# Optimization experiments

Measured on AMD Instinct MI355X. Metric: run time of the kernel, lower is better.

Reference implementation:

```python
import jax, jax.numpy as jnp
import numpy as np

N_NODES = 50000
N_EDGES = 800000
N_GRAPHS = 64
IN_CH = 128
HID = 128
PROC_X = 128
Q_DIM = 768
PROC_Q = 128
OUT_CH = 32


def setup_inputs() -> dict:
    key = jax.random.key(0)
    ks = jax.random.split(key, 16)
    inp = {
        "x": jax.random.normal(ks[0], (N_NODES, IN_CH), dtype=jnp.float32),
        "edge_index": jax.random.randint(ks[1], (2, N_EDGES), 0, N_NODES, dtype=jnp.int64),
        "batch": jnp.sort(jax.random.randint(ks[2], (N_NODES,), 0, N_GRAPHS, dtype=jnp.int64)),
        "question_embedding": jax.random.normal(ks[3], (N_GRAPHS, Q_DIM), dtype=jnp.float32),
    }
    s = 1.0 / np.sqrt(HID)
    inp["W0"] = jax.random.uniform(ks[4], (IN_CH, HID), minval=-s, maxval=s)
    inp["b0"] = jnp.zeros((HID,), jnp.float32)
    inp["W1"] = jax.random.uniform(ks[5], (HID, HID), minval=-s, maxval=s)
    inp["b1"] = jnp.zeros((HID,), jnp.float32)
    inp["W2"] = jax.random.uniform(ks[6], (HID, PROC_X), minval=-s, maxval=s)
    inp["b2"] = jnp.zeros((PROC_X,), jnp.float32)
    inp["fc0_w"] = jax.random.uniform(ks[7], (Q_DIM, PROC_Q), minval=-s, maxval=s)
    inp["fc0_b"] = jnp.zeros((PROC_Q,), jnp.float32)
    inp["fc1_w"] = jax.random.uniform(ks[8], (PROC_X + PROC_Q, HID), minval=-s, maxval=s)
    inp["fc1_b"] = jnp.zeros((HID,), jnp.float32)
    inp["fc2_w"] = jax.random.uniform(ks[9], (HID, OUT_CH), minval=-s, maxval=s)
    inp["fc2_b"] = jnp.zeros((OUT_CH,), jnp.float32)
    return inp


def _gcn_norm(edge_index, n_nodes):
    """Add self-loops and compute symmetric GCN normalization per edge."""
    loop = jnp.arange(n_nodes, dtype=edge_index.dtype)
    src = jnp.concatenate([edge_index[0], loop])
    dst = jnp.concatenate([edge_index[1], loop])
    ones = jnp.ones_like(dst, dtype=jnp.float32)
    deg = jax.ops.segment_sum(ones, dst, num_segments=n_nodes)
    dinv = jnp.where(deg > 0, jax.lax.rsqrt(deg), 0.0)
    norm = dinv[src] * dinv[dst]  # [E+N]
    return src, dst, norm


def _gcn_conv(x, src, dst, norm, W, b):
    h = x @ W                                # [N, F_out]
    msg = h[src] * norm[:, None]             # gather + scale  [E+N, F_out]
    agg = jax.ops.segment_sum(msg, dst, num_segments=x.shape[0])
    return agg + b


def reference(x, edge_index, batch, question_embedding,
              W0, b0, W1, b1, W2, b2,
              fc0_w, fc0_b, fc1_w, fc1_b, fc2_w, fc2_b):
    n = x.shape[0]
    src, dst, norm = _gcn_norm(edge_index, n)
    h = jax.nn.relu(_gcn_conv(x, src, dst, norm, W0, b0))
    h = jax.nn.relu(_gcn_conv(h, src, dst, norm, W1, b1))
    h = jax.nn.relu(_gcn_conv(h, src, dst, norm, W2, b2))
    q = jax.nn.relu(question_embedding @ fc0_w + fc0_b)  # [G, PROC_Q]
    q_exp = q[batch]                                      # [N, PROC_Q]
    combined = jnp.concatenate([h, q_exp], axis=1)
    out = jax.nn.relu(combined @ fc1_w + fc1_b)
    out = out @ fc2_w + fc2_b
    return out
```

## Files before the change

kernel.cpp:

```cpp
#include <hip/hip_runtime.h>
#include <hip/hip_bf16.h>

#define N_NODES 50000
#define N_EDGES 800000
#define N_GRAPHS 64
#define LSTR 136

typedef __attribute__((ext_vector_type(4))) short s4v;
typedef __attribute__((ext_vector_type(8))) short s8v;
typedef __attribute__((ext_vector_type(16))) float f16v;

struct HL { short hi, lo; };

__device__ inline HL bsplit(float f) {
    HL r;
    unsigned u = __float_as_uint(f);
    unsigned rh = (u + 0x7FFFu + ((u >> 16) & 1u)) >> 16;
    r.hi = (short)rh;
    float fh = __uint_as_float(rh << 16);
    float fl = f - fh;
    unsigned u2 = __float_as_uint(fl);
    unsigned rl = (u2 + 0x7FFFu + ((u2 >> 16) & 1u)) >> 16;
    r.lo = (short)rl;
    return r;
}

__device__ inline unsigned short f2bf(float f) {
    unsigned u = __float_as_uint(f);
    return (unsigned short)((u + 0x7FFFu + ((u >> 16) & 1u)) >> 16);
}

__device__ inline float bflo(unsigned u) { return __uint_as_float(u << 16); }
__device__ inline float bfhi(unsigned u) { return __uint_as_float(u & 0xFFFF0000u); }


__global__ void k_hist(const int* __restrict__ ei, int* __restrict__ cnt,
                       int* __restrict__ rank, int E) {
    int e = blockIdx.x * 256 + threadIdx.x;
    if (e < E) rank[e] = atomicAdd(&cnt[ei[E + e]], 1);
}

__global__ __launch_bounds__(512) void k_scan_a(const int* __restrict__ cnt,
                                                int* __restrict__ rowptr,
                                                int* __restrict__ bsum,
                                                float* __restrict__ dinv, int n) {
    __shared__ int s[512];
    int t = threadIdx.x;
    int i = blockIdx.x * 512 + t;
    int v = (i < n) ? cnt[i] : 0;
    if (i < n) dinv[i] = rsqrtf((float)(v + 1));
    int pv = (v + 7) & ~7;
    s[t] = pv;
    __syncthreads();
    for (int d = 1; d < 512; d <<= 1) {
        int x = (t >= d) ? s[t - d] : 0;
        __syncthreads();
        s[t] += x;
        __syncthreads();
    }
    if (i < n) rowptr[i] = s[t] - pv;
    if (t == 511) bsum[blockIdx.x] = s[511];
}

__global__ __launch_bounds__(512) void k_scan_c(int* __restrict__ rowptr,
                                                const int* __restrict__ bsum,
                                                int n, int nb) {
    __shared__ int sb[128];
    int t = threadIdx.x;
    if (t < 128) sb[t] = (t < nb) ? bsum[t] : 0;
    __syncthreads();
    for (int d = 1; d < 128; d <<= 1) {
        int x = 0;
        if (t < 128 && t >= d) x = sb[t - d];
        __syncthreads();
        if (t < 128) sb[t] += x;
        __syncthreads();
    }
    int add = (blockIdx.x > 0) ? sb[blockIdx.x - 1] : 0;
    int i = blockIdx.x * 512 + t;
    if (i < n) rowptr[i] += add;
    if (i == 0) rowptr[n] = sb[nb - 1];
}

__global__ void k_fill_csr(const int* __restrict__ ei, const int* __restrict__ rowptr,
                           const int* __restrict__ rank,
                           unsigned short* __restrict__ colA, int E) {
    int e = blockIdx.x * 256 + threadIdx.x;
    if (e >= E) return;
    colA[rowptr[ei[E + e]] + rank[e]] = (unsigned short)ei[e];
}

__global__ __launch_bounds__(512) void k_prep(const float* __restrict__ qe,
                                              const float* __restrict__ fc0w,
                                              const float* __restrict__ fc0b,
                                              const float* __restrict__ fc1w,
                                              const float* __restrict__ fc1b,
                                              const float* __restrict__ W0,
                                              const float* __restrict__ W1,
                                              const float* __restrict__ W2,
                                              const float* __restrict__ fc2w,
                                              short* __restrict__ WH,
                                              short* __restrict__ WL,
                                              int* __restrict__ cntz,
                                              unsigned* __restrict__ Hsd,
                                              unsigned short* __restrict__ colA,
                                              float* __restrict__ qq) {
    int b = blockIdx.x, tid = threadIdx.x;
    if (b >= 225) {
        int idx = (b - 225) * 512 + tid;
        if (idx < 143752) {
            uint4 p;
            p.x = p.y = p.z = p.w = 0xC350C350u;
            ((uint4*)colA)[idx] = p;
        }
        return;
    }
    if (b >= 200) {
        int idx = (b - 200) * 512 + tid;
        if (idx < 12504) ((int4*)cntz)[idx] = make_int4(0, 0, 0, 0);
        if (b == 200 && tid < 64) Hsd[(unsigned)N_NODES * 64u + tid] = 0u;
        return;
    }
    if (b >= 64) {
        int i = (b - 64) * 512 + tid;
        float val;
        int dst;
        if (i < 65536) {
            int mat = i >> 14, off = i & 16383;
            int k = off >> 7, n = off & 127;
            const float* src = (mat == 0) ? W0 : (mat == 1) ? W1 : (mat == 2) ? W2 : fc1w;
            val = src[k * 128 + n];
            dst = mat * 16384 + n * 128 + k;
        } else {
            int off = i - 65536;
            int k = off >> 5, n = off & 31;
            val = fc2w[k * 32 + n];
            dst = 65536 + n * 128 + k;
        }
        HL r = bsplit(val);
        WH[dst] = r.hi;
        WL[dst] = r.lo;
        return;
    }
    __shared__ float qs[768];
    __shared__ float red[512];
    __shared__ float ql[128];
    const float* fc1bot = fc1w + 128 * 128;
    int g = b;
    for (int i = tid; i < 768; i += 512) qs[i] = qe[g * 768 + i];
    __syncthreads();
    int j = tid & 127, sl = tid >> 7;
    int kb = sl * 192;
    float a0 = 0, a1 = 0, a2 = 0, a3 = 0;
    for (int k = 0; k < 192; k += 4) {
        a0 += qs[kb + k + 0] * fc0w[(kb + k + 0) * 128 + j];
        a1 += qs[kb + k + 1] * fc0w[(kb + k + 1) * 128 + j];
        a2 += qs[kb + k + 2] * fc0w[(kb + k + 2) * 128 + j];
        a3 += qs[kb + k + 3] * fc0w[(kb + k + 3) * 128 + j];
    }
    red[tid] = (a0 + a1) + (a2 + a3);
    __syncthreads();
    if (tid < 128)
        ql[tid] = fmaxf(((red[tid] + red[tid + 128]) + (red[tid + 256] + red[tid + 384]))
                        + fc0b[tid], 0.f);
    __syncthreads();
    kb = sl * 32;
    float b0 = 0, b1 = 0;
    for (int k = 0; k < 32; k += 2) {
        b0 += ql[kb + k + 0] * fc1bot[(kb + k + 0) * 128 + j];
        b1 += ql[kb + k + 1] * fc1bot[(kb + k + 1) * 128 + j];
    }
    red[tid] = b0 + b1;
    __syncthreads();
    if (tid < 128)
        qq[g * 128 + tid] = ((red[tid] + red[tid + 128]) + (red[tid + 256] + red[tid + 384]))
                            + fc1b[tid];
}

__global__ __launch_bounds__(256) void k_gather(const unsigned* __restrict__ Hs,
                                                const int* __restrict__ rowptr,
                                                const unsigned short* __restrict__ colA,
                                                const float* __restrict__ dinv,
                                                const float* __restrict__ bias,
                                                unsigned* __restrict__ GH, int n) {
    int node = __builtin_amdgcn_readfirstlane(blockIdx.x * 4 + (threadIdx.x >> 6));
    if (node >= n) return;
    int l = threadIdx.x & 63;
    int e0 = __builtin_amdgcn_readfirstlane(rowptr[node]);
    int e1 = __builtin_amdgcn_readfirstlane(rowptr[node + 1]);
    float a0 = 0.f, a1 = 0.f;
    for (int e = e0; e < e1; e += 8) {
        uint4 cw = *(const uint4*)(colA + e);
        const unsigned* r0 = Hs + (cw.x & 0xFFFFu) * 64u;
        const unsigned* r1 = Hs + (cw.x >> 16) * 64u;
        const unsigned* r2 = Hs + (cw.y & 0xFFFFu) * 64u;
        const unsigned* r3 = Hs + (cw.y >> 16) * 64u;
        const unsigned* r4 = Hs + (cw.z & 0xFFFFu) * 64u;
        const unsigned* r5 = Hs + (cw.z >> 16) * 64u;
        const unsigned* r6 = Hs + (cw.w & 0xFFFFu) * 64u;
        const unsigned* r7 = Hs + (cw.w >> 16) * 64u;
        unsigned u0 = r0[l], u1 = r1[l], u2 = r2[l], u3 = r3[l];
        unsigned u4 = r4[l], u5 = r5[l], u6 = r6[l], u7 = r7[l];
        a0 += ((bflo(u0) + bflo(u1)) + (bflo(u2) + bflo(u3)))
            + ((bflo(u4) + bflo(u5)) + (bflo(u6) + bflo(u7)));
        a1 += ((bfhi(u0) + bfhi(u1)) + (bfhi(u2) + bfhi(u3)))
            + ((bfhi(u4) + bfhi(u5)) + (bfhi(u6) + bfhi(u7)));
    }
    float di = dinv[node];
    unsigned uh = Hs[(unsigned)node * 64u + l];
    float2 bb = ((const float2*)bias)[l];
    float o0 = fmaxf((a0 + bflo(uh)) * di + bb.x, 0.f);
    float o1 = fmaxf((a1 + bfhi(uh)) * di + bb.y, 0.f);
    GH[(unsigned)node * 64u + l] = (unsigned)f2bf(o0) | ((unsigned)f2bf(o1) << 16);
}

template <int SPLITIN>
__global__ __launch_bounds__(128) void gemm_mf(const float* __restrict__ A32,
                                               const unsigned short* __restrict__ GHin,
                                               const short* __restrict__ WTh,
                                               const short* __restrict__ WTl,
                                               const float* __restrict__ dinv,
                                               unsigned short* __restrict__ oHs,
                                               int nrows) {
    __shared__ short Ah[32 * LSTR];
    const int tid = threadIdx.x;
    const int row0 = blockIdx.x * 32;

    if (SPLITIN == 0) {
        #pragma unroll
        for (int i = 0; i < 8; ++i) {
            int u = i * 128 + tid;
            int r = u >> 5, c4 = u & 31;
            int gr = row0 + r;
            float4 v = make_float4(0.f, 0.f, 0.f, 0.f);
            if (gr < nrows) v = ((const float4*)A32)[(size_t)gr * 32 + c4];
            s4v h4 = {(short)f2bf(v.x), (short)f2bf(v.y), (short)f2bf(v.z), (short)f2bf(v.w)};
            *(s4v*)&Ah[r * LSTR + c4 * 4] = h4;
        }
    } else {
        #pragma unroll
        for (int i = 0; i < 4; ++i) {
            int u = i * 128 + tid;
            int r = u >> 4, j = u & 15;
            int gr = row0 + r;
            s8v h8 = {};
            if (gr < nrows) h8 = *(const s8v*)&GHin[(size_t)gr * 128 + j * 8];
            *(s8v*)&Ah[r * LSTR + j * 8] = h8;
        }
    }
    __syncthreads();

    const int wv = tid >> 6, lane = tid & 63;
    const int m = lane & 31, half = lane >> 5;
    const int c0 = wv * 64 + m;
    f16v acc0 = {0.f}, acc1 = {0.f};
    #pragma unroll
    for (int ks = 0; ks < 8; ++ks) {
        int ko = ks * 16 + half * 8;
        s8v ah  = *(const s8v*)&Ah[m * LSTR + ko];
        s8v bh0 = *(const s8v*)&WTh[(size_t)c0 * 128 + ko];
        s8v bl0 = *(const s8v*)&WTl[(size_t)c0 * 128 + ko];
        s8v bh1 = *(const s8v*)&WTh[(size_t)(c0 + 32) * 128 + ko];
        s8v bl1 = *(const s8v*)&WTl[(size_t)(c0 + 32) * 128 + ko];
        acc0 = __builtin_amdgcn_mfma_f32_32x32x16_bf16(ah, bh0, acc0, 0, 0, 0);
        acc0 = __builtin_amdgcn_mfma_f32_32x32x16_bf16(ah, bl0, acc0, 0, 0, 0);
        acc1 = __builtin_amdgcn_mfma_f32_32x32x16_bf16(ah, bh1, acc1, 0, 0, 0);
        acc1 = __builtin_amdgcn_mfma_f32_32x32x16_bf16(ah, bl1, acc1, 0, 0, 0);
    }

    #pragma unroll
    for (int reg = 0; reg < 16; ++reg) {
        int rl = (reg & 3) + 8 * (reg >> 2) + 4 * half;
        int gr = row0 + rl;
        if (gr >= nrows) continue;
        float sc = dinv[gr];
        oHs[(size_t)gr * 128 + c0]      = f2bf(acc0[reg] * sc);
        oHs[(size_t)gr * 128 + c0 + 32] = f2bf(acc1[reg] * sc);
    }
}

__global__ __launch_bounds__(128) void k_fc12(const unsigned short* __restrict__ GHin,
                                              const short* __restrict__ W1h,
                                              const short* __restrict__ W1l,
                                              const short* __restrict__ W2h,
                                              const short* __restrict__ W2l,
                                              const float* __restrict__ qq,
                                              const int* __restrict__ batch,
                                              const float* __restrict__ bias,
                                              float* __restrict__ out, int nrows) {
    __shared__ short Ph[32 * LSTR], Pl[32 * LSTR];
    __shared__ float red[32 * 33];
    const int tid = threadIdx.x;
    const int row0 = blockIdx.x * 32;

    #pragma unroll
    for (int i = 0; i < 4; ++i) {
        int u = i * 128 + tid;
        int r = u >> 4, j = u & 15;
        int gr = row0 + r;
        s8v h8 = {};
        if (gr < nrows) h8 = *(const s8v*)&GHin[(size_t)gr * 128 + j * 8];
        *(s8v*)&Ph[r * LSTR + j * 8] = h8;
    }
    __syncthreads();

    const int wv = tid >> 6, lane = tid & 63;
    const int m = lane & 31, half = lane >> 5;
    const int c0 = wv * 64 + m;
    f16v acc0 = {0.f}, acc1 = {0.f};
    #pragma unroll
    for (int ks = 0; ks < 8; ++ks) {
        int ko = ks * 16 + half * 8;
        s8v ah  = *(const s8v*)&Ph[m * LSTR + ko];
        s8v bh0 = *(const s8v*)&W1h[(size_t)c0 * 128 + ko];
        s8v bl0 = *(const s8v*)&W1l[(size_t)c0 * 128 + ko];
        s8v bh1 = *(const s8v*)&W1h[(size_t)(c0 + 32) * 128 + ko];
        s8v bl1 = *(const s8v*)&W1l[(size_t)(c0 + 32) * 128 + ko];
        acc0 = __builtin_amdgcn_mfma_f32_32x32x16_bf16(ah, bh0, acc0, 0, 0, 0);
        acc0 = __builtin_amdgcn_mfma_f32_32x32x16_bf16(ah, bl0, acc0, 0, 0, 0);
        acc1 = __builtin_amdgcn_mfma_f32_32x32x16_bf16(ah, bh1, acc1, 0, 0, 0);
        acc1 = __builtin_amdgcn_mfma_f32_32x32x16_bf16(ah, bl1, acc1, 0, 0, 0);
    }
    __syncthreads();

    #pragma unroll
    for (int reg = 0; reg < 16; ++reg) {
        int rl = (reg & 3) + 8 * (reg >> 2) + 4 * half;
        int gr = row0 + rl;
        int g = (gr < nrows) ? batch[gr] : 0;
        float q0 = qq[(size_t)g * 128 + c0];
        float q1 = qq[(size_t)g * 128 + c0 + 32];
        float v0 = fmaxf(acc0[reg] + q0, 0.f);
        float v1 = fmaxf(acc1[reg] + q1, 0.f);
        HL p0 = bsplit(v0), p1 = bsplit(v1);
        Ph[rl * LSTR + c0] = p0.hi;
        Pl[rl * LSTR + c0] = p0.lo;
        Ph[rl * LSTR + c0 + 32] = p1.hi;
        Pl[rl * LSTR + c0 + 32] = p1.lo;
    }
    __syncthreads();

    f16v acc2 = {0.f};
    #pragma unroll
    for (int ks = 0; ks < 4; ++ks) {
        int ko = wv * 64 + ks * 16 + half * 8;
        s8v ah = *(const s8v*)&Ph[m * LSTR + ko];
        s8v al = *(const s8v*)&Pl[m * LSTR + ko];
        s8v bh = *(const s8v*)&W2h[(size_t)m * 128 + ko];
        s8v bl = *(const s8v*)&W2l[(size_t)m * 128 + ko];
        acc2 = __builtin_amdgcn_mfma_f32_32x32x16_bf16(ah, bh, acc2, 0, 0, 0);
        acc2 = __builtin_amdgcn_mfma_f32_32x32x16_bf16(ah, bl, acc2, 0, 0, 0);
        acc2 = __builtin_amdgcn_mfma_f32_32x32x16_bf16(al, bh, acc2, 0, 0, 0);
    }
    if (wv == 1) {
        #pragma unroll
        for (int reg = 0; reg < 16; ++reg) {
            int rl = (reg & 3) + 8 * (reg >> 2) + 4 * half;
            red[rl * 33 + m] = acc2[reg];
        }
    }
    __syncthreads();
    if (wv == 0) {
        #pragma unroll
        for (int reg = 0; reg < 16; ++reg) {
            int rl = (reg & 3) + 8 * (reg >> 2) + 4 * half;
            int gr = row0 + rl;
            if (gr < nrows)
                out[(size_t)gr * 32 + m] = acc2[reg] + red[rl * 33 + m] + bias[m];
        }
    }
}


extern "C" void kernel_launch(void* const* d_in, const int* in_sizes, int n_in,
                              void* d_out, int out_size, void* d_ws, size_t ws_size,
                              hipStream_t stream) {
    const float* x    = (const float*)d_in[0];
    const int*   ei   = (const int*)d_in[1];
    const int*   batch= (const int*)d_in[2];
    const float* qe   = (const float*)d_in[3];
    const float* W0   = (const float*)d_in[4];
    const float* b0   = (const float*)d_in[5];
    const float* W1   = (const float*)d_in[6];
    const float* b1   = (const float*)d_in[7];
    const float* W2   = (const float*)d_in[8];
    const float* b2   = (const float*)d_in[9];
    const float* fc0w = (const float*)d_in[10];
    const float* fc0b = (const float*)d_in[11];
    const float* fc1w = (const float*)d_in[12];
    const float* fc1b = (const float*)d_in[13];
    const float* fc2w = (const float*)d_in[14];
    const float* fc2b = (const float*)d_in[15];
    float* out = (float*)d_out;

    float* WS = (float*)d_ws;
    unsigned short* HS = (unsigned short*)WS;
    unsigned short* GH = (unsigned short*)(WS + 3200064);
    float* DINV = WS + 6400064;
    float* QQ   = WS + 6450080;
    int*   CNT  = (int*)(WS + 6458272);
    int*   ROWPTR = (int*)(WS + 6508288);
    int*   RANK = (int*)(WS + 6558304);
    unsigned short* COL = (unsigned short*)(WS + 7358304);
    int*   BSUM = (int*)(WS + 7933312);
    short* WTH  = (short*)(WS + 7933440);
    short* WTL  = WTH + 69632;

    const int N = N_NODES, E = N_EDGES;
    const int eb = (E + 255) / 256;
    const int sb = (N + 511) / 512;
    const int gg = (N + 31) / 32;
    const int gat = (N + 3) / 4;

    k_prep<<<506, 512, 0, stream>>>(qe, fc0w, fc0b, fc1w, fc1b, W0, W1, W2, fc2w,
                                    WTH, WTL, CNT, (unsigned*)HS, COL, QQ);
    k_hist<<<eb, 256, 0, stream>>>(ei, CNT, RANK, E);
    k_scan_a<<<sb, 512, 0, stream>>>(CNT, ROWPTR, BSUM, DINV, N);
    k_scan_c<<<sb, 512, 0, stream>>>(ROWPTR, BSUM, N, sb);
    k_fill_csr<<<eb, 256, 0, stream>>>(ei, ROWPTR, RANK, COL, E);

    gemm_mf<0><<<gg, 128, 0, stream>>>(x, nullptr, WTH, WTL, DINV, HS, N);
    k_gather<<<gat, 256, 0, stream>>>((const unsigned*)HS, ROWPTR, COL, DINV, b0,
                                      (unsigned*)GH, N);
    gemm_mf<1><<<gg, 128, 0, stream>>>(nullptr, GH, WTH + 16384, WTL + 16384, DINV, HS, N);
    k_gather<<<gat, 256, 0, stream>>>((const unsigned*)HS, ROWPTR, COL, DINV, b1,
                                      (unsigned*)GH, N);
    gemm_mf<1><<<gg, 128, 0, stream>>>(nullptr, GH, WTH + 32768, WTL + 32768, DINV, HS, N);
    k_gather<<<gat, 256, 0, stream>>>((const unsigned*)HS, ROWPTR, COL, DINV, b2,
                                      (unsigned*)GH, N);

    k_fc12<<<gg, 128, 0, stream>>>(GH, WTH + 49152, WTL + 49152,
                                   WTH + 65536, WTL + 65536,
                                   QQ, batch, fc2b, out, N);
}
```

Baseline: 333.7 us.

## Fuse neighbor gather with following dense GEMM into one kernel per layer

Merges each gather/aggregation pass with the next layer's MFMA GEMM (or the final fc1/fc2 head). A 256-thread block gathers 32 nodes into LDS, then four waves each compute a 32-column slice. Ping-pong H buffers replace the intermediate GH array. This removes the global write and re-read of the aggregated features and three kernel launches. In exchange, gather parallelism per block is coarser: each wave walks 8 nodes serially, which may hurt latency hiding.

```diff
diff --git a/kernel.cpp b/kernel.cpp
--- a/kernel.cpp
+++ b/kernel.cpp
@@ -103,6 +103,7 @@
                                               short* __restrict__ WL,
                                               int* __restrict__ cntz,
                                               unsigned* __restrict__ Hsd,
+                                              unsigned* __restrict__ Hsd2,
                                               unsigned short* __restrict__ colA,
                                               float* __restrict__ qq) {
     int b = blockIdx.x, tid = threadIdx.x;
@@ -118,7 +119,10 @@
     if (b >= 200) {
         int idx = (b - 200) * 512 + tid;
         if (idx < 12504) ((int4*)cntz)[idx] = make_int4(0, 0, 0, 0);
-        if (b == 200 && tid < 64) Hsd[(unsigned)N_NODES * 64u + tid] = 0u;
+        if (b == 200 && tid < 64) {
+            Hsd[(unsigned)N_NODES * 64u + tid] = 0u;
+            Hsd2[(unsigned)N_NODES * 64u + tid] = 0u;
+        }
         return;
     }
     if (b >= 64) {
@@ -177,46 +181,7 @@
                             + fc1b[tid];
 }
 
-__global__ __launch_bounds__(256) void k_gather(const unsigned* __restrict__ Hs,
-                                                const int* __restrict__ rowptr,
-                                                const unsigned short* __restrict__ colA,
-                                                const float* __restrict__ dinv,
-                                                const float* __restrict__ bias,
-                                                unsigned* __restrict__ GH, int n) {
-    int node = __builtin_amdgcn_readfirstlane(blockIdx.x * 4 + (threadIdx.x >> 6));
-    if (node >= n) return;
-    int l = threadIdx.x & 63;
-    int e0 = __builtin_amdgcn_readfirstlane(rowptr[node]);
-    int e1 = __builtin_amdgcn_readfirstlane(rowptr[node + 1]);
-    float a0 = 0.f, a1 = 0.f;
-    for (int e = e0; e < e1; e += 8) {
-        uint4 cw = *(const uint4*)(colA + e);
-        const unsigned* r0 = Hs + (cw.x & 0xFFFFu) * 64u;
-        const unsigned* r1 = Hs + (cw.x >> 16) * 64u;
-        const unsigned* r2 = Hs + (cw.y & 0xFFFFu) * 64u;
-        const unsigned* r3 = Hs + (cw.y >> 16) * 64u;
-        const unsigned* r4 = Hs + (cw.z & 0xFFFFu) * 64u;
-        const unsigned* r5 = Hs + (cw.z >> 16) * 64u;
-        const unsigned* r6 = Hs + (cw.w & 0xFFFFu) * 64u;
-        const unsigned* r7 = Hs + (cw.w >> 16) * 64u;
-        unsigned u0 = r0[l], u1 = r1[l], u2 = r2[l], u3 = r3[l];
-        unsigned u4 = r4[l], u5 = r5[l], u6 = r6[l], u7 = r7[l];
-        a0 += ((bflo(u0) + bflo(u1)) + (bflo(u2) + bflo(u3)))
-            + ((bflo(u4) + bflo(u5)) + (bflo(u6) + bflo(u7)));
-        a1 += ((bfhi(u0) + bfhi(u1)) + (bfhi(u2) + bfhi(u3)))
-            + ((bfhi(u4) + bfhi(u5)) + (bfhi(u6) + bfhi(u7)));
-    }
-    float di = dinv[node];
-    unsigned uh = Hs[(unsigned)node * 64u + l];
-    float2 bb = ((const float2*)bias)[l];
-    float o0 = fmaxf((a0 + bflo(uh)) * di + bb.x, 0.f);
-    float o1 = fmaxf((a1 + bfhi(uh)) * di + bb.y, 0.f);
-    GH[(unsigned)node * 64u + l] = (unsigned)f2bf(o0) | ((unsigned)f2bf(o1) << 16);
-}
-
-template <int SPLITIN>
 __global__ __launch_bounds__(128) void gemm_mf(const float* __restrict__ A32,
-                                               const unsigned short* __restrict__ GHin,
                                                const short* __restrict__ WTh,
                                                const short* __restrict__ WTl,
                                                const float* __restrict__ dinv,
@@ -226,27 +191,15 @@
     const int tid = threadIdx.x;
     const int row0 = blockIdx.x * 32;
 
-    if (SPLITIN == 0) {
-        #pragma unroll
-        for (int i = 0; i < 8; ++i) {
-            int u = i * 128 + tid;
-            int r = u >> 5, c4 = u & 31;
-            int gr = row0 + r;
-            float4 v = make_float4(0.f, 0.f, 0.f, 0.f);
-            if (gr < nrows) v = ((const float4*)A32)[(size_t)gr * 32 + c4];
-            s4v h4 = {(short)f2bf(v.x), (short)f2bf(v.y), (short)f2bf(v.z), (short)f2bf(v.w)};
-            *(s4v*)&Ah[r * LSTR + c4 * 4] = h4;
-        }
-    } else {
-        #pragma unroll
-        for (int i = 0; i < 4; ++i) {
-            int u = i * 128 + tid;
-            int r = u >> 4, j = u & 15;
-            int gr = row0 + r;
-            s8v h8 = {};
-            if (gr < nrows) h8 = *(const s8v*)&GHin[(size_t)gr * 128 + j * 8];
-            *(s8v*)&Ah[r * LSTR + j * 8] = h8;
-        }
+    #pragma unroll
+    for (int i = 0; i < 8; ++i) {
+        int u = i * 128 + tid;
+        int r = u >> 5, c4 = u & 31;
+        int gr = row0 + r;
+        float4 v = make_float4(0.f, 0.f, 0.f, 0.f);
+        if (gr < nrows) v = ((const float4*)A32)[(size_t)gr * 32 + c4];
+        s4v h4 = {(short)f2bf(v.x), (short)f2bf(v.y), (short)f2bf(v.z), (short)f2bf(v.w)};
+        *(s4v*)&Ah[r * LSTR + c4 * 4] = h4;
     }
     __syncthreads();
 
@@ -279,94 +232,127 @@
     }
 }
 
-__global__ __launch_bounds__(128) void k_fc12(const unsigned short* __restrict__ GHin,
-                                              const short* __restrict__ W1h,
-                                              const short* __restrict__ W1l,
-                                              const short* __restrict__ W2h,
-                                              const short* __restrict__ W2l,
-                                              const float* __restrict__ qq,
-                                              const int* __restrict__ batch,
-                                              const float* __restrict__ bias,
-                                              float* __restrict__ out, int nrows) {
-    __shared__ short Ph[32 * LSTR], Pl[32 * LSTR];
-    __shared__ float red[32 * 33];
+template <int FC>
+__global__ __launch_bounds__(256) void k_gg(const unsigned* __restrict__ Hs,
+                                            const int* __restrict__ rowptr,
+                                            const unsigned short* __restrict__ colA,
+                                            const float* __restrict__ dinv,
+                                            const float* __restrict__ bias,
+                                            const short* __restrict__ WTh,
+                                            const short* __restrict__ WTl,
+                                            const short* __restrict__ W2h,
+                                            const short* __restrict__ W2l,
+                                            const float* __restrict__ qq,
+                                            const int* __restrict__ batch,
+                                            const float* __restrict__ fc2b,
+                                            unsigned short* __restrict__ oHs,
+                                            float* __restrict__ out,
+                                            int n) {
+    __shared__ short Ah[32 * LSTR];
+    __shared__ short Pl[FC ? 32 * LSTR : 1];
+    __shared__ float red[FC ? 3 * 32 * 33 : 1];
     const int tid = threadIdx.x;
     const int row0 = blockIdx.x * 32;
-
-    #pragma unroll
-    for (int i = 0; i < 4; ++i) {
-        int u = i * 128 + tid;
-        int r = u >> 4, j = u & 15;
-        int gr = row0 + r;
-        s8v h8 = {};
-        if (gr < nrows) h8 = *(const s8v*)&GHin[(size_t)gr * 128 + j * 8];
-        *(s8v*)&Ph[r * LSTR + j * 8] = h8;
-    }
-    __syncthreads();
-
-    const int wv = tid >> 6, lane = tid & 63;
-    const int m = lane & 31, half = lane >> 5;
-    const int c0 = wv * 64 + m;
-    f16v acc0 = {0.f}, acc1 = {0.f};
+    const int wv = tid >> 6, l = tid & 63;
+    const int m = l & 31, half = l >> 5;
+
+    const float2 bb = ((const float2*)bias)[l];
+    for (int i = 0; i < 8; ++i) {
+        int r = wv * 8 + i;
+        int node = row0 + r;
+        unsigned pack = 0;
+        if (node < n) {
+            int e0 = __builtin_amdgcn_readfirstlane(rowptr[node]);
+            int e1 = __builtin_amdgcn_readfirstlane(rowptr[node + 1]);
+            float a0 = 0.f, a1 = 0.f;
+            for (int e = e0; e < e1; e += 8) {
+                uint4 cw = *(const uint4*)(colA + e);
+                unsigned u0 = Hs[(cw.x & 0xFFFFu) * 64u + l];
+                unsigned u1 = Hs[(cw.x >> 16) * 64u + l];
+                unsigned u2 = Hs[(cw.y & 0xFFFFu) * 64u + l];
+                unsigned u3 = Hs[(cw.y >> 16) * 64u + l];
+                unsigned u4 = Hs[(cw.z & 0xFFFFu) * 64u + l];
+                unsigned u5 = Hs[(cw.z >> 16) * 64u + l];
+                unsigned u6 = Hs[(cw.w & 0xFFFFu) * 64u + l];
+                unsigned u7 = Hs[(cw.w >> 16) * 64u + l];
+                a0 += ((bflo(u0) + bflo(u1)) + (bflo(u2) + bflo(u3)))
+                    + ((bflo(u4) + bflo(u5)) + (bflo(u6) + bflo(u7)));
+                a1 += ((bfhi(u0) + bfhi(u1)) + (bfhi(u2) + bfhi(u3)))
+                    + ((bfhi(u4) + bfhi(u5)) + (bfhi(u6) + bfhi(u7)));
+            }
+            float di = dinv[node];
+            unsigned uh = Hs[(unsigned)node * 64u + l];
+            float o0 = fmaxf((a0 + bflo(uh)) * di + bb.x, 0.f);
+            float o1 = fmaxf((a1 + bfhi(uh)) * di + bb.y, 0.f);
+            pack = (unsigned)f2bf(o0) | ((unsigned)f2bf(o1) << 16);
+        }
+        ((unsigned*)Ah)[r * 68 + l] = pack;
+    }
+    __syncthreads();
+
+    const int c0 = wv * 32 + m;
+    f16v acc = {0.f};
     #pragma unroll
     for (int ks = 0; ks < 8; ++ks) {
         int ko = ks * 16 + half * 8;
-        s8v ah  = *(const s8v*)&Ph[m * LSTR + ko];
-        s8v bh0 = *(const s8v*)&W1h[(size_t)c0 * 128 + ko];
-        s8v bl0 = *(const s8v*)&W1l[(size_t)c0 * 128 + ko];
-        s8v bh1 = *(const s8v*)&W1h[(size_t)(c0 + 32) * 128 + ko];
-        s8v bl1 = *(const s8v*)&W1l[(size_t)(c0 + 32) * 128 + ko];
-        acc0 = __builtin_amdgcn_mfma_f32_32x32x16_bf16(ah, bh0, acc0, 0, 0, 0);
-        acc0 = __builtin_amdgcn_mfma_f32_32x32x16_bf16(ah, bl0, acc0, 0, 0, 0);
-        acc1 = __builtin_amdgcn_mfma_f32_32x32x16_bf16(ah, bh1, acc1, 0, 0, 0);
-        acc1 = __builtin_amdgcn_mfma_f32_32x32x16_bf16(ah, bl1, acc1, 0, 0, 0);
-    }
-    __syncthreads();
-
-    #pragma unroll
-    for (int reg = 0; reg < 16; ++reg) {
-        int rl = (reg & 3) + 8 * (reg >> 2) + 4 * half;
-        int gr = row0 + rl;
-        int g = (gr < nrows) ? batch[gr] : 0;
-        float q0 = qq[(size_t)g * 128 + c0];
-        float q1 = qq[(size_t)g * 128 + c0 + 32];
-        float v0 = fmaxf(acc0[reg] + q0, 0.f);
-        float v1 = fmaxf(acc1[reg] + q1, 0.f);
-        HL p0 = bsplit(v0), p1 = bsplit(v1);
-        Ph[rl * LSTR + c0] = p0.hi;
-        Pl[rl * LSTR + c0] = p0.lo;
-        Ph[rl * LSTR + c0 + 32] = p1.hi;
-        Pl[rl * LSTR + c0 + 32] = p1.lo;
-    }
-    __syncthreads();
-
-    f16v acc2 = {0.f};
-    #pragma unroll
-    for (int ks = 0; ks < 4; ++ks) {
-        int ko = wv * 64 + ks * 16 + half * 8;
-        s8v ah = *(const s8v*)&Ph[m * LSTR + ko];
-        s8v al = *(const s8v*)&Pl[m * LSTR + ko];
-        s8v bh = *(const s8v*)&W2h[(size_t)m * 128 + ko];
-        s8v bl = *(const s8v*)&W2l[(size_t)m * 128 + ko];
-        acc2 = __builtin_amdgcn_mfma_f32_32x32x16_bf16(ah, bh, acc2, 0, 0, 0);
-        acc2 = __builtin_amdgcn_mfma_f32_32x32x16_bf16(ah, bl, acc2, 0, 0, 0);
-        acc2 = __builtin_amdgcn_mfma_f32_32x32x16_bf16(al, bh, acc2, 0, 0, 0);
-    }
-    if (wv == 1) {
-        #pragma unroll
-        for (int reg = 0; reg < 16; ++reg) {
-            int rl = (reg & 3) + 8 * (reg >> 2) + 4 * half;
-            red[rl * 33 + m] = acc2[reg];
-        }
-    }
-    __syncthreads();
-    if (wv == 0) {
+        s8v ah = *(const s8v*)&Ah[m * LSTR + ko];
+        s8v bh = *(const s8v*)&WTh[(size_t)c0 * 128 + ko];
+        s8v bl = *(const s8v*)&WTl[(size_t)c0 * 128 + ko];
+        acc = __builtin_amdgcn_mfma_f32_32x32x16_bf16(ah, bh, acc, 0, 0, 0);
+        acc = __builtin_amdgcn_mfma_f32_32x32x16_bf16(ah, bl, acc, 0, 0, 0);
+    }
+
+    if (FC == 0) {
         #pragma unroll
         for (int reg = 0; reg < 16; ++reg) {
             int rl = (reg & 3) + 8 * (reg >> 2) + 4 * half;
             int gr = row0 + rl;
-            if (gr < nrows)
-                out[(size_t)gr * 32 + m] = acc2[reg] + red[rl * 33 + m] + bias[m];
+            if (gr >= n) continue;
+            oHs[(size_t)gr * 128 + c0] = f2bf(acc[reg] * dinv[gr]);
+        }
+    } else {
+        __syncthreads();
+        #pragma unroll
+        for (int reg = 0; reg < 16; ++reg) {
+            int rl = (reg & 3) + 8 * (reg >> 2) + 4 * half;
+            int gr = row0 + rl;
+            int g = (gr < n) ? batch[gr] : 0;
+            float v = fmaxf(acc[reg] + qq[(size_t)g * 128 + c0], 0.f);
+            HL p = bsplit(v);
+            Ah[rl * LSTR + c0] = p.hi;
+            Pl[rl * LSTR + c0] = p.lo;
+        }
+        __syncthreads();
+        f16v acc2 = {0.f};
+        #pragma unroll
+        for (int ks = 0; ks < 2; ++ks) {
+            int ko = wv * 32 + ks * 16 + half * 8;
+            s8v ah = *(const s8v*)&Ah[m * LSTR + ko];
+            s8v al = *(const s8v*)&Pl[m * LSTR + ko];
+            s8v bh = *(const s8v*)&W2h[(size_t)m * 128 + ko];
+            s8v bl = *(const s8v*)&W2l[(size_t)m * 128 + ko];
+            acc2 = __builtin_amdgcn_mfma_f32_32x32x16_bf16(ah, bh, acc2, 0, 0, 0);
+            acc2 = __builtin_amdgcn_mfma_f32_32x32x16_bf16(ah, bl, acc2, 0, 0, 0);
+            acc2 = __builtin_amdgcn_mfma_f32_32x32x16_bf16(al, bh, acc2, 0, 0, 0);
+        }
+        if (wv > 0) {
+            #pragma unroll
+            for (int reg = 0; reg < 16; ++reg) {
+                int rl = (reg & 3) + 8 * (reg >> 2) + 4 * half;
+                red[(wv - 1) * 1056 + rl * 33 + m] = acc2[reg];
+            }
+        }
+        __syncthreads();
+        if (wv == 0) {
+            #pragma unroll
+            for (int reg = 0; reg < 16; ++reg) {
+                int rl = (reg & 3) + 8 * (reg >> 2) + 4 * half;
+                int gr = row0 + rl;
+                if (gr < n)
+                    out[(size_t)gr * 32 + m] = acc2[reg]
+                        + (red[rl * 33 + m] + red[1056 + rl * 33 + m])
+                        + red[2112 + rl * 33 + m] + fc2b[m];
+            }
         }
     }
 }
@@ -394,42 +380,38 @@
     float* out = (float*)d_out;
 
     float* WS = (float*)d_ws;
-    unsigned short* HS = (unsigned short*)WS;
-    unsigned short* GH = (unsigned short*)(WS + 3200064);
-    float* DINV = WS + 6400064;
-    float* QQ   = WS + 6450080;
-    int*   CNT  = (int*)(WS + 6458272);
-    int*   ROWPTR = (int*)(WS + 6508288);
-    int*   RANK = (int*)(WS + 6558304);
-    unsigned short* COL = (unsigned short*)(WS + 7358304);
-    int*   BSUM = (int*)(WS + 7933312);
-    short* WTH  = (short*)(WS + 7933440);
+    unsigned short* HS  = (unsigned short*)WS;
+    unsigned short* HS2 = (unsigned short*)(WS + 3200064);
+    float* DINV = WS + 6400128;
+    float* QQ   = WS + 6450144;
+    int*   CNT  = (int*)(WS + 6458336);
+    int*   ROWPTR = (int*)(WS + 6508352);
+    int*   RANK = (int*)(WS + 6558368);
+    unsigned short* COL = (unsigned short*)(WS + 7358368);
+    int*   BSUM = (int*)(WS + 7933376);
+    short* WTH  = (short*)(WS + 7933504);
     short* WTL  = WTH + 69632;
 
     const int N = N_NODES, E = N_EDGES;
     const int eb = (E + 255) / 256;
     const int sb = (N + 511) / 512;
     const int gg = (N + 31) / 32;
-    const int gat = (N + 3) / 4;
 
     k_prep<<<506, 512, 0, stream>>>(qe, fc0w, fc0b, fc1w, fc1b, W0, W1, W2, fc2w,
-                                    WTH, WTL, CNT, (unsigned*)HS, COL, QQ);
+                                    WTH, WTL, CNT, (unsigned*)HS, (unsigned*)HS2, COL, QQ);
     k_hist<<<eb, 256, 0, stream>>>(ei, CNT, RANK, E);
     k_scan_a<<<sb, 512, 0, stream>>>(CNT, ROWPTR, BSUM, DINV, N);
     k_scan_c<<<sb, 512, 0, stream>>>(ROWPTR, BSUM, N, sb);
     k_fill_csr<<<eb, 256, 0, stream>>>(ei, ROWPTR, RANK, COL, E);
 
-    gemm_mf<0><<<gg, 128, 0, stream>>>(x, nullptr, WTH, WTL, DINV, HS, N);
-    k_gather<<<gat, 256, 0, stream>>>((const unsigned*)HS, ROWPTR, COL, DINV, b0,
-                                      (unsigned*)GH, N);
-    gemm_mf<1><<<gg, 128, 0, stream>>>(nullptr, GH, WTH + 16384, WTL + 16384, DINV, HS, N);
-    k_gather<<<gat, 256, 0, stream>>>((const unsigned*)HS, ROWPTR, COL, DINV, b1,
-                                      (unsigned*)GH, N);
-    gemm_mf<1><<<gg, 128, 0, stream>>>(nullptr, GH, WTH + 32768, WTL + 32768, DINV, HS, N);
-    k_gather<<<gat, 256, 0, stream>>>((const unsigned*)HS, ROWPTR, COL, DINV, b2,
-                                      (unsigned*)GH, N);
-
-    k_fc12<<<gg, 128, 0, stream>>>(GH, WTH + 49152, WTL + 49152,
-                                   WTH + 65536, WTL + 65536,
-                                   QQ, batch, fc2b, out, N);
-}
+    gemm_mf<<<gg, 128, 0, stream>>>(x, WTH, WTL, DINV, HS, N);
+    k_gg<0><<<gg, 256, 0, stream>>>((const unsigned*)HS, ROWPTR, COL, DINV, b0,
+                                    WTH + 16384, WTL + 16384, nullptr, nullptr,
+                                    nullptr, nullptr, nullptr, HS2, nullptr, N);
+    k_gg<0><<<gg, 256, 0, stream>>>((const unsigned*)HS2, ROWPTR, COL, DINV, b1,
+                                    WTH + 32768, WTL + 32768, nullptr, nullptr,
+                                    nullptr, nullptr, nullptr, HS, nullptr, N);
+    k_gg<1><<<gg, 256, 0, stream>>>((const unsigned*)HS, ROWPTR, COL, DINV, b2,
+                                    WTH + 49152, WTL + 49152, WTH + 65536, WTL + 65536,
+                                    QQ, batch, fc2b, nullptr, out, N);
+}
```

Result: faster. 323.1 us (-3.2%).

## Split gather into feature-column phases with four edges per wavefront

Applied to the files above, without the earlier changes.

The per-node gather kernel is restructured so each grid phase handles a 16-column slice of the bf16-packed feature row. Each wavefront processes four edges at once, one per 16-lane group, over eight consecutive nodes, and combines partial sums with cross-lane shuffles. This shrinks the working set of each phase so gathered rows are more likely to hit in cache. In exchange it issues more, smaller (64-byte) loads, adds shuffle reductions, and rereads the column indices four times.

```diff
diff --git a/kernel.cpp b/kernel.cpp
--- a/kernel.cpp
+++ b/kernel.cpp
@@ -177,41 +177,50 @@
                             + fc1b[tid];
 }
 
-__global__ __launch_bounds__(256) void k_gather(const unsigned* __restrict__ Hs,
-                                                const int* __restrict__ rowptr,
-                                                const unsigned short* __restrict__ colA,
-                                                const float* __restrict__ dinv,
-                                                const float* __restrict__ bias,
-                                                unsigned* __restrict__ GH, int n) {
-    int node = __builtin_amdgcn_readfirstlane(blockIdx.x * 4 + (threadIdx.x >> 6));
-    if (node >= n) return;
-    int l = threadIdx.x & 63;
-    int e0 = __builtin_amdgcn_readfirstlane(rowptr[node]);
-    int e1 = __builtin_amdgcn_readfirstlane(rowptr[node + 1]);
-    float a0 = 0.f, a1 = 0.f;
-    for (int e = e0; e < e1; e += 8) {
-        uint4 cw = *(const uint4*)(colA + e);
-        const unsigned* r0 = Hs + (cw.x & 0xFFFFu) * 64u;
-        const unsigned* r1 = Hs + (cw.x >> 16) * 64u;
-        const unsigned* r2 = Hs + (cw.y & 0xFFFFu) * 64u;
-        const unsigned* r3 = Hs + (cw.y >> 16) * 64u;
-        const unsigned* r4 = Hs + (cw.z & 0xFFFFu) * 64u;
-        const unsigned* r5 = Hs + (cw.z >> 16) * 64u;
-        const unsigned* r6 = Hs + (cw.w & 0xFFFFu) * 64u;
-        const unsigned* r7 = Hs + (cw.w >> 16) * 64u;
-        unsigned u0 = r0[l], u1 = r1[l], u2 = r2[l], u3 = r3[l];
-        unsigned u4 = r4[l], u5 = r5[l], u6 = r6[l], u7 = r7[l];
-        a0 += ((bflo(u0) + bflo(u1)) + (bflo(u2) + bflo(u3)))
-            + ((bflo(u4) + bflo(u5)) + (bflo(u6) + bflo(u7)));
-        a1 += ((bfhi(u0) + bfhi(u1)) + (bfhi(u2) + bfhi(u3)))
-            + ((bfhi(u4) + bfhi(u5)) + (bfhi(u6) + bfhi(u7)));
-    }
-    float di = dinv[node];
-    unsigned uh = Hs[(unsigned)node * 64u + l];
-    float2 bb = ((const float2*)bias)[l];
-    float o0 = fmaxf((a0 + bflo(uh)) * di + bb.x, 0.f);
-    float o1 = fmaxf((a1 + bfhi(uh)) * di + bb.y, 0.f);
-    GH[(unsigned)node * 64u + l] = (unsigned)f2bf(o0) | ((unsigned)f2bf(o1) << 16);
+__global__ __launch_bounds__(256) void k_gat(const unsigned* __restrict__ Hs,
+                                             const int* __restrict__ rowptr,
+                                             const unsigned short* __restrict__ colA,
+                                             const float* __restrict__ dinv,
+                                             const float* __restrict__ bias,
+                                             unsigned* __restrict__ GH,
+                                             int n, int NB) {
+    const int phase = blockIdx.x / NB;
+    const int nb = blockIdx.x - phase * NB;
+    const int wv = threadIdx.x >> 6, l = threadIdx.x & 63;
+    const int d = l & 15;
+    const unsigned* base = Hs + phase * 16 + d;
+    const float2 bb = ((const float2*)bias)[phase * 16 + d];
+
+    for (int i = 0; i < 8; ++i) {
+        int node = nb * 32 + wv * 8 + i;
+        if (node >= n) return;
+        int e0 = __builtin_amdgcn_readfirstlane(rowptr[node]);
+        int e1 = __builtin_amdgcn_readfirstlane(rowptr[node + 1]);
+        float a0 = 0.f, a1 = 0.f;
+        for (int e = e0; e < e1; e += 8) {
+            uint4 cw = *(const uint4*)(colA + e);
+            unsigned s0 = (l & 32) ? cw.y : cw.x;
+            unsigned i0 = (l & 16) ? (s0 >> 16) : (s0 & 0xFFFFu);
+            unsigned s1 = (l & 32) ? cw.w : cw.z;
+            unsigned i1 = (l & 16) ? (s1 >> 16) : (s1 & 0xFFFFu);
+            unsigned u0 = base[i0 * 64u];
+            unsigned u1 = base[i1 * 64u];
+            a0 += bflo(u0) + bflo(u1);
+            a1 += bfhi(u0) + bfhi(u1);
+        }
+        a0 += __shfl_down(a0, 32);
+        a1 += __shfl_down(a1, 32);
+        a0 += __shfl_down(a0, 16);
+        a1 += __shfl_down(a1, 16);
+        if (l < 16) {
+            float di = dinv[node];
+            unsigned uh = base[(unsigned)node * 64u];
+            float o0 = fmaxf((a0 + bflo(uh)) * di + bb.x, 0.f);
+            float o1 = fmaxf((a1 + bfhi(uh)) * di + bb.y, 0.f);
+            GH[(unsigned)node * 64u + phase * 16 + d] =
+                (unsigned)f2bf(o0) | ((unsigned)f2bf(o1) << 16);
+        }
+    }
 }
 
 template <int SPLITIN>
@@ -410,7 +419,7 @@
     const int eb = (E + 255) / 256;
     const int sb = (N + 511) / 512;
     const int gg = (N + 31) / 32;
-    const int gat = (N + 3) / 4;
+    const int NB = (N + 31) / 32;
 
     k_prep<<<506, 512, 0, stream>>>(qe, fc0w, fc0b, fc1w, fc1b, W0, W1, W2, fc2w,
                                     WTH, WTL, CNT, (unsigned*)HS, COL, QQ);
@@ -420,14 +429,14 @@
     k_fill_csr<<<eb, 256, 0, stream>>>(ei, ROWPTR, RANK, COL, E);
 
     gemm_mf<0><<<gg, 128, 0, stream>>>(x, nullptr, WTH, WTL, DINV, HS, N);
-    k_gather<<<gat, 256, 0, stream>>>((const unsigned*)HS, ROWPTR, COL, DINV, b0,
-                                      (unsigned*)GH, N);
+    k_gat<<<4 * NB, 256, 0, stream>>>((const unsigned*)HS, ROWPTR, COL, DINV, b0,
+                                      (unsigned*)GH, N, NB);
     gemm_mf<1><<<gg, 128, 0, stream>>>(nullptr, GH, WTH + 16384, WTL + 16384, DINV, HS, N);
-    k_gather<<<gat, 256, 0, stream>>>((const unsigned*)HS, ROWPTR, COL, DINV, b1,
-                                      (unsigned*)GH, N);
+    k_gat<<<4 * NB, 256, 0, stream>>>((const unsigned*)HS, ROWPTR, COL, DINV, b1,
+                                      (unsigned*)GH, N, NB);
     gemm_mf<1><<<gg, 128, 0, stream>>>(nullptr, GH, WTH + 32768, WTL + 32768, DINV, HS, N);
-    k_gather<<<gat, 256, 0, stream>>>((const unsigned*)HS, ROWPTR, COL, DINV, b2,
-                                      (unsigned*)GH, N);
+    k_gat<<<4 * NB, 256, 0, stream>>>((const unsigned*)HS, ROWPTR, COL, DINV, b2,
+                                      (unsigned*)GH, N, NB);
 
     k_fc12<<<gg, 128, 0, stream>>>(GH, WTH + 49152, WTL + 49152,
                                    WTH + 65536, WTL + 65536,
```

New measurement: 444.1 us. 33.1% more time.
